# Kernel optimization log

Hardware: AMD Instinct MI355X
Metric: run time of the kernel (lower is better)

## Reference

```python
import jax, jax.numpy as jnp
import numpy as np

N = 50000
E = 800000
IN_C, HID_C, OUT_C = 128, 128, 64


def setup_inputs() -> dict:
    key = jax.random.key(0)
    k_x, k_e, k_w1, k_w2 = jax.random.split(key, 4)
    x = jax.random.normal(k_x, (N, IN_C), dtype=jnp.float32)
    edge_index = jax.random.randint(k_e, (2, E), 0, N, dtype=jnp.int64)
    # glorot-ish init scale
    W1 = jax.random.normal(k_w1, (IN_C, HID_C), dtype=jnp.float32) * (1.0 / np.sqrt(IN_C))
    b1 = jnp.zeros((HID_C,), dtype=jnp.float32)
    W2 = jax.random.normal(k_w2, (HID_C, OUT_C), dtype=jnp.float32) * (1.0 / np.sqrt(HID_C))
    b2 = jnp.zeros((OUT_C,), dtype=jnp.float32)
    return {"x": x, "edge_index": edge_index, "W1": W1, "b1": b1, "W2": W2, "b2": b2}


def _gcn_norm(edge_index, num_nodes):
    # PyG gcn_norm with add_self_loops=True: deg over destination (col), sym norm
    loops = jnp.arange(num_nodes, dtype=edge_index.dtype)
    src = jnp.concatenate([edge_index[0], loops])
    dst = jnp.concatenate([edge_index[1], loops])
    deg = jax.ops.segment_sum(jnp.ones_like(dst, dtype=jnp.float32), dst, num_segments=num_nodes)
    dinv = jnp.where(deg > 0, jax.lax.rsqrt(deg), 0.0)
    norm = dinv[src] * dinv[dst]  # [E+N]
    return src, dst, norm


def _gcn_conv(x, src, dst, norm, W, b, num_nodes):
    h = x @ W                              # [N, out]
    msg = h[src] * norm[:, None]           # [E+N, out] gather + scale
    agg = jax.ops.segment_sum(msg, dst, num_segments=num_nodes)  # scatter-add
    return agg + b


def reference(x, edge_index, W1, b1, W2, b2):
    num_nodes = x.shape[0]
    src, dst, norm = _gcn_norm(edge_index, num_nodes)
    h = _gcn_conv(x, src, dst, norm, W1, b1, num_nodes)
    h = jax.nn.relu(h)
    out = _gcn_conv(h, src, dst, norm, W2, b2, num_nodes)
    return out
```

## Files before the change

kernel.cpp:

```cpp
#include <hip/hip_runtime.h>
#include <hip/hip_bf16.h>


#define IN_C 128
#define HID_C 128
#define OUT_C 64
#define BKT_SH 8
#define BKT_NODES 256
#define CHUNK 4096
#define CAPB 6144
#define OVF_CAP 65536

typedef float f32x4 __attribute__((ext_vector_type(4)));
typedef short bf16x8 __attribute__((ext_vector_type(8)));

__device__ inline unsigned short f2bf_rtn(float f) {
  unsigned u = __float_as_uint(f);
  unsigned r = u + 0x7fffu + ((u >> 16) & 1u);
  return (unsigned short)(r >> 16);
}
__device__ inline unsigned pack_bf2(float a, float b) {
  return (unsigned)f2bf_rtn(a) | ((unsigned)f2bf_rtn(b) << 16);
}

__global__ __launch_bounds__(256) void wt_zero_kernel(
    const float* __restrict__ W1, const float* __restrict__ W2,
    short* __restrict__ w1t, short* __restrict__ w2t,
    int* __restrict__ zbase, int zints) {
  int i = blockIdx.x * 256 + threadIdx.x;
  if (i < zints) zbase[i] = 0;
  if (i < IN_C * HID_C) {
    int n = i >> 7, k = i & 127;
    w1t[i] = (short)f2bf_rtn(W1[k * HID_C + n]);
  }
  if (i < HID_C * OUT_C) {
    int n = i >> 7, k = i & 127;
    w2t[i] = (short)f2bf_rtn(W2[k * OUT_C + n]);
  }
}

__global__ __launch_bounds__(256) void phase1_bin_kernel(
    const int* __restrict__ ei, unsigned* __restrict__ pairs,
    int* __restrict__ bcnt, uint2* __restrict__ ovf, int* __restrict__ ovf_cnt,
    int* __restrict__ ovfb, int E, int K) {
  __shared__ unsigned buf[CHUNK];
  __shared__ int hist[256];
  __shared__ int lofs[256];
  __shared__ int cur[256];
  __shared__ int gbase[256];
  int t = threadIdx.x;
  int base_e = blockIdx.x * CHUNK;
  int cnt_e = E - base_e;
  if (cnt_e > CHUNK) cnt_e = CHUNK;

  hist[t] = 0;
  __syncthreads();

  for (int i = t; i < cnt_e; i += 256)
    atomicAdd(&hist[ei[E + base_e + i] >> BKT_SH], 1);
  __syncthreads();

  int v = hist[t];
  int lane = t & 63, wid = t >> 6;
  int inc = v;
  #pragma unroll
  for (int off = 1; off < 64; off <<= 1) {
    int u = __shfl_up(inc, off, 64);
    if (lane >= off) inc += u;
  }
  __shared__ int ws4[4];
  if (lane == 63) ws4[wid] = inc;
  __syncthreads();
  if (t == 0) {
    int a = ws4[0], b = ws4[1], c = ws4[2];
    ws4[0] = 0; ws4[1] = a; ws4[2] = a + b; ws4[3] = a + b + c;
  }
  __syncthreads();
  int excl = ws4[wid] + inc - v;
  lofs[t] = excl;
  cur[t] = excl;
  if (t < K && v > 0) gbase[t] = atomicAdd(&bcnt[t], v);
  __syncthreads();

  for (int i = t; i < cnt_e; i += 256) {
    int src = ei[base_e + i];
    int dst = ei[E + base_e + i];
    int b = dst >> BKT_SH;
    int pos = atomicAdd(&cur[b], 1);
    buf[pos] = (unsigned)src | ((unsigned)(dst & (BKT_NODES - 1)) << 16) |
               ((unsigned)b << 24);
  }
  __syncthreads();

  for (int i = t; i < cnt_e; i += 256) {
    unsigned w = buf[i];
    int b = w >> 24;
    int g = gbase[b] + (i - lofs[b]);
    if (g < CAPB) {
      pairs[(size_t)b * CAPB + g] = w;
    } else {
      int oi = atomicAdd(ovf_cnt, 1);
      if (oi < OVF_CAP) {
        unsigned dst = (unsigned)(b << BKT_SH) | ((w >> 16) & 0xFFu);
        ovf[oi] = make_uint2(w & 0xFFFFu, dst);
        atomicAdd(&ovfb[b], 1);
      }
    }
  }
}

__global__ __launch_bounds__(256) void bucket_scan_kernel(
    const int* __restrict__ bcnt, const int* __restrict__ ovfb,
    int* __restrict__ bucket_base, int* __restrict__ rowstart, int K, int N) {
  int t = threadIdx.x;
  int tot = 0;
  if (t < K) {
    int c = bcnt[t];
    tot = (c < CAPB ? c : CAPB) + ovfb[t];
  }
  int lane = t & 63, wid = t >> 6;
  int inc = tot;
  #pragma unroll
  for (int off = 1; off < 64; off <<= 1) {
    int u = __shfl_up(inc, off, 64);
    if (lane >= off) inc += u;
  }
  __shared__ int ws4[4];
  if (lane == 63) ws4[wid] = inc;
  __syncthreads();
  if (t == 0) {
    int a = ws4[0], b = ws4[1], c = ws4[2];
    ws4[0] = 0; ws4[1] = a; ws4[2] = a + b; ws4[3] = a + b + c;
  }
  __syncthreads();
  int excl = ws4[wid] + inc - tot;
  if (t <= K) bucket_base[t] = excl;
  if (t == K) rowstart[N] = excl;
}

__global__ __launch_bounds__(256) void phase2_csr_kernel(
    const unsigned* __restrict__ pairs, const int* __restrict__ bcnt,
    const uint2* __restrict__ ovf, const int* __restrict__ ovf_cnt,
    const int* __restrict__ bucket_base, int* __restrict__ rowstart,
    float* __restrict__ dinv, unsigned short* __restrict__ csr, int N) {
  int b = blockIdx.x;
  int t = threadIdx.x;
  __shared__ int hist[BKT_NODES];
  __shared__ int cur[BKT_NODES];
  hist[t] = 0;
  __syncthreads();

  int cnt = bcnt[b];
  if (cnt > CAPB) cnt = CAPB;
  const unsigned* reg = pairs + (size_t)b * CAPB;

  for (int i = t; i < cnt; i += 256)
    atomicAdd(&hist[(reg[i] >> 16) & 0xFFu], 1);
  int oc = *ovf_cnt;
  if (oc > OVF_CAP) oc = OVF_CAP;
  for (int i = t; i < oc; i += 256) {
    uint2 p = ovf[i];
    if ((int)(p.y >> BKT_SH) == b) atomicAdd(&hist[p.y & (BKT_NODES - 1)], 1);
  }
  __syncthreads();

  int v = hist[t];
  int lane = t & 63, wid = t >> 6;
  int inc = v;
  #pragma unroll
  for (int off = 1; off < 64; off <<= 1) {
    int u = __shfl_up(inc, off, 64);
    if (lane >= off) inc += u;
  }
  __shared__ int ws4[4];
  if (lane == 63) ws4[wid] = inc;
  __syncthreads();
  if (t == 0) {
    int a = ws4[0], bb = ws4[1], c = ws4[2];
    ws4[0] = 0; ws4[1] = a; ws4[2] = a + bb; ws4[3] = a + bb + c;
  }
  __syncthreads();
  int excl = ws4[wid] + inc - v;

  int base = bucket_base[b];
  int node = b * BKT_NODES + t;
  if (node < N) {
    rowstart[node] = base + excl;
    dinv[node] = rsqrtf((float)(v + 1));
  }
  cur[t] = base + excl;
  __syncthreads();

  for (int i = t; i < cnt; i += 256) {
    unsigned w = reg[i];
    int pos = atomicAdd(&cur[(w >> 16) & 0xFFu], 1);
    csr[pos] = (unsigned short)(w & 0xffffu);
  }
  for (int i = t; i < oc; i += 256) {
    uint2 p = ovf[i];
    if ((int)(p.y >> BKT_SH) == b) {
      int pos = atomicAdd(&cur[p.y & (BKT_NODES - 1)], 1);
      csr[pos] = (unsigned short)p.x;
    }
  }
}

template <int COUT, bool ABF16>
__global__ __launch_bounds__(256) void mfma_gemm_kernel(
    const void* __restrict__ Xv, const short* __restrict__ Wt,
    const float* __restrict__ dinv, unsigned short* __restrict__ H, int ntiles) {
  int lane = threadIdx.x & 63;
  int tile = blockIdx.x * 4 + (threadIdx.x >> 6);
  if (tile >= ntiles) return;
  constexpr int NT = COUT / 16;

  int arow = tile * 16 + (lane & 15);
  int kch = (lane >> 4) * 8;

  bf16x8 afrag[4];
  if (ABF16) {
    const bf16x8* Xb = (const bf16x8*)Xv;
    #pragma unroll
    for (int kt = 0; kt < 4; ++kt)
      afrag[kt] = Xb[(size_t)arow * 16 + (kt * 32 + kch) / 8];
  } else {
    const float4* Xf = (const float4*)Xv;
    #pragma unroll
    for (int kt = 0; kt < 4; ++kt) {
      float4 f0 = Xf[(size_t)arow * 32 + (kt * 32 + kch) / 4];
      float4 f1 = Xf[(size_t)arow * 32 + (kt * 32 + kch) / 4 + 1];
      bf16x8 a;
      a[0] = (short)f2bf_rtn(f0.x); a[1] = (short)f2bf_rtn(f0.y);
      a[2] = (short)f2bf_rtn(f0.z); a[3] = (short)f2bf_rtn(f0.w);
      a[4] = (short)f2bf_rtn(f1.x); a[5] = (short)f2bf_rtn(f1.y);
      a[6] = (short)f2bf_rtn(f1.z); a[7] = (short)f2bf_rtn(f1.w);
      afrag[kt] = a;
    }
  }

  const bf16x8* W8 = (const bf16x8*)Wt;
  f32x4 zero = {0.f, 0.f, 0.f, 0.f};
  f32x4 acc[NT];
  #pragma unroll
  for (int ct = 0; ct < NT; ++ct) acc[ct] = zero;

  #pragma unroll
  for (int ct = 0; ct < NT; ++ct) {
    int bcol = ct * 16 + (lane & 15);
    #pragma unroll
    for (int kt = 0; kt < 4; ++kt) {
      bf16x8 b = W8[bcol * 16 + (kt * 32 + kch) / 8];
      acc[ct] = __builtin_amdgcn_mfma_f32_16x16x32_bf16(afrag[kt], b, acc[ct], 0, 0, 0);
    }
  }

  int r0 = tile * 16 + (lane >> 4) * 4;
  float di[4];
  #pragma unroll
  for (int j = 0; j < 4; ++j) di[j] = dinv[r0 + j];
  #pragma unroll
  for (int ct = 0; ct < NT; ++ct) {
    #pragma unroll
    for (int j = 0; j < 4; ++j)
      H[(size_t)(r0 + j) * COUT + ct * 16 + (lane & 15)] = f2bf_rtn(acc[ct][j] * di[j]);
  }
}

template <int C, bool RELU, bool OUT_BF16>
__global__ __launch_bounds__(256) void agg_bf16_kernel(
    const unsigned short* __restrict__ Hs, const int* __restrict__ rowstart,
    const unsigned short* __restrict__ csr, const float* __restrict__ dinv,
    const float* __restrict__ bias, void* __restrict__ out, int n) {
  constexpr int TPN = C / 8;
  constexpr int NPB = 256 / TPN;
  int lane = threadIdx.x % TPN;
  int node = blockIdx.x * NPB + threadIdx.x / TPN;
  if (node >= n) return;

  const uint4* H4 = reinterpret_cast<const uint4*>(Hs);
  int s = rowstart[node];
  int e = rowstart[node + 1];

  float acc[8];
  {
    uint4 v = H4[(size_t)node * TPN + lane];
    acc[0] = __uint_as_float(v.x << 16);
    acc[1] = __uint_as_float(v.x & 0xffff0000u);
    acc[2] = __uint_as_float(v.y << 16);
    acc[3] = __uint_as_float(v.y & 0xffff0000u);
    acc[4] = __uint_as_float(v.z << 16);
    acc[5] = __uint_as_float(v.z & 0xffff0000u);
    acc[6] = __uint_as_float(v.w << 16);
    acc[7] = __uint_as_float(v.w & 0xffff0000u);
  }

  int p = s;
  for (; p + 1 < e; p += 2) {
    int s0 = csr[p];
    int s1 = csr[p + 1];
    uint4 v0 = H4[(size_t)s0 * TPN + lane];
    uint4 v1 = H4[(size_t)s1 * TPN + lane];
    acc[0] += __uint_as_float(v0.x << 16);
    acc[1] += __uint_as_float(v0.x & 0xffff0000u);
    acc[2] += __uint_as_float(v0.y << 16);
    acc[3] += __uint_as_float(v0.y & 0xffff0000u);
    acc[4] += __uint_as_float(v0.z << 16);
    acc[5] += __uint_as_float(v0.z & 0xffff0000u);
    acc[6] += __uint_as_float(v0.w << 16);
    acc[7] += __uint_as_float(v0.w & 0xffff0000u);
    acc[0] += __uint_as_float(v1.x << 16);
    acc[1] += __uint_as_float(v1.x & 0xffff0000u);
    acc[2] += __uint_as_float(v1.y << 16);
    acc[3] += __uint_as_float(v1.y & 0xffff0000u);
    acc[4] += __uint_as_float(v1.z << 16);
    acc[5] += __uint_as_float(v1.z & 0xffff0000u);
    acc[6] += __uint_as_float(v1.w << 16);
    acc[7] += __uint_as_float(v1.w & 0xffff0000u);
  }
  if (p < e) {
    int s0 = csr[p];
    uint4 v0 = H4[(size_t)s0 * TPN + lane];
    acc[0] += __uint_as_float(v0.x << 16);
    acc[1] += __uint_as_float(v0.x & 0xffff0000u);
    acc[2] += __uint_as_float(v0.y << 16);
    acc[3] += __uint_as_float(v0.y & 0xffff0000u);
    acc[4] += __uint_as_float(v0.z << 16);
    acc[5] += __uint_as_float(v0.z & 0xffff0000u);
    acc[6] += __uint_as_float(v0.w << 16);
    acc[7] += __uint_as_float(v0.w & 0xffff0000u);
  }

  float di = dinv[node];
  float4 b0 = reinterpret_cast<const float4*>(bias)[lane * 2];
  float4 b1 = reinterpret_cast<const float4*>(bias)[lane * 2 + 1];
  float r[8];
  r[0] = fmaf(acc[0], di, b0.x);
  r[1] = fmaf(acc[1], di, b0.y);
  r[2] = fmaf(acc[2], di, b0.z);
  r[3] = fmaf(acc[3], di, b0.w);
  r[4] = fmaf(acc[4], di, b1.x);
  r[5] = fmaf(acc[5], di, b1.y);
  r[6] = fmaf(acc[6], di, b1.z);
  r[7] = fmaf(acc[7], di, b1.w);
  if (RELU) {
    #pragma unroll
    for (int j = 0; j < 8; ++j) r[j] = fmaxf(r[j], 0.f);
  }
  if (OUT_BF16) {
    uint4 o;
    o.x = pack_bf2(r[0], r[1]);
    o.y = pack_bf2(r[2], r[3]);
    o.z = pack_bf2(r[4], r[5]);
    o.w = pack_bf2(r[6], r[7]);
    reinterpret_cast<uint4*>(out)[(size_t)node * TPN + lane] = o;
  } else {
    float4* o4 = reinterpret_cast<float4*>(out) + (size_t)node * (C / 4);
    o4[lane * 2] = make_float4(r[0], r[1], r[2], r[3]);
    o4[lane * 2 + 1] = make_float4(r[4], r[5], r[6], r[7]);
  }
}

extern "C" void kernel_launch(void* const* d_in, const int* in_sizes, int n_in,
                              void* d_out, int out_size, void* d_ws, size_t ws_size,
                              hipStream_t stream) {
  const float* x  = (const float*)d_in[0];
  const int*   ei = (const int*)d_in[1];
  const float* W1 = (const float*)d_in[2];
  const float* b1 = (const float*)d_in[3];
  const float* W2 = (const float*)d_in[4];
  const float* b2 = (const float*)d_in[5];
  float* out = (float*)d_out;

  const int N = in_sizes[0] / IN_C;
  const int E = in_sizes[1] / 2;
  const int K = (N + BKT_NODES - 1) >> BKT_SH;
  const int NTILES = (N + 15) / 16;

  char* ws = (char*)d_ws;
  size_t off = 0;
  auto alloc = [&](size_t bytes) -> void* {
    void* p = ws + off;
    off += (bytes + 255) & ~(size_t)255;
    return p;
  };
  int* bcnt    = (int*)alloc((size_t)K * 4);
  int* ovf_cnt = (int*)alloc(4);
  int* ovfb    = (int*)alloc((size_t)K * 4);
  size_t zero_bytes = off;
  const int zints = (int)(zero_bytes / 4);

  int*   bucket_base = (int*)  alloc((size_t)(K + 1) * 4);
  int*   rowstart    = (int*)  alloc((size_t)(N + 1) * 4);
  float* dinv        = (float*)alloc((size_t)N * 4);
  unsigned* pairs    = (unsigned*)alloc((size_t)K * CAPB * 4);
  uint2* ovf         = (uint2*)alloc((size_t)OVF_CAP * 8);
  unsigned short* csr = (unsigned short*)alloc((size_t)E * 2);
  unsigned short* hs  = (unsigned short*)alloc((size_t)N * HID_C * 2);
  unsigned short* x2  = (unsigned short*)alloc((size_t)N * HID_C * 2);
  short* w1t         = (short*)alloc((size_t)IN_C * HID_C * 2);
  short* w2t         = (short*)alloc((size_t)HID_C * OUT_C * 2);

  int wt_threads = zints > IN_C * HID_C ? zints : IN_C * HID_C;
  wt_zero_kernel<<<(wt_threads + 255) / 256, 256, 0, stream>>>(
      W1, W2, w1t, w2t, (int*)ws, zints);
  phase1_bin_kernel<<<(E + CHUNK - 1) / CHUNK, 256, 0, stream>>>(
      ei, pairs, bcnt, ovf, ovf_cnt, ovfb, E, K);
  bucket_scan_kernel<<<1, 256, 0, stream>>>(bcnt, ovfb, bucket_base, rowstart, K, N);
  phase2_csr_kernel<<<K, 256, 0, stream>>>(
      pairs, bcnt, ovf, ovf_cnt, bucket_base, rowstart, dinv, csr, N);

  mfma_gemm_kernel<HID_C, false><<<(NTILES + 3) / 4, 256, 0, stream>>>(
      x, w1t, dinv, hs, NTILES);
  agg_bf16_kernel<HID_C, true, true><<<(N + 15) / 16, 256, 0, stream>>>(
      hs, rowstart, csr, dinv, b1, x2, N);

  mfma_gemm_kernel<OUT_C, true><<<(NTILES + 3) / 4, 256, 0, stream>>>(
      x2, w2t, dinv, hs, NTILES);
  agg_bf16_kernel<OUT_C, false, false><<<(N + 31) / 32, 256, 0, stream>>>(
      hs, rowstart, csr, dinv, b2, out, N);
}
```

Before: 123.5 us.

## Slice aggregation kernels by feature columns and use nontemporal csr loads and stores

The aggregation kernels now split each node's feature row into 32-byte column slices, with consecutive blocks handling the same node range for different slices. Each block gathers only a narrow slice of H across 128 nodes. The intent is to shrink each block's gather working set and improve L2 locality. The cost is that every slice re-reads rowstart and csr. The csr loads and output stores also become nontemporal to avoid polluting the cache.

```diff
diff --git a/kernel.cpp b/kernel.cpp
--- a/kernel.cpp
+++ b/kernel.cpp
@@ -12,6 +12,7 @@
 #define OVF_CAP 65536
 
 typedef float f32x4 __attribute__((ext_vector_type(4)));
+typedef unsigned u32x4 __attribute__((ext_vector_type(4)));
 typedef short bf16x8 __attribute__((ext_vector_type(8)));
 
 __device__ inline unsigned short f2bf_rtn(float f) {
@@ -266,24 +267,27 @@
   }
 }
 
-template <int C, bool RELU, bool OUT_BF16>
-__global__ __launch_bounds__(256) void agg_bf16_kernel(
+template <int C, int SLICES, bool RELU, bool OUT_BF16>
+__global__ __launch_bounds__(256) void agg_sliced_kernel(
     const unsigned short* __restrict__ Hs, const int* __restrict__ rowstart,
     const unsigned short* __restrict__ csr, const float* __restrict__ dinv,
     const float* __restrict__ bias, void* __restrict__ out, int n) {
-  constexpr int TPN = C / 8;
-  constexpr int NPB = 256 / TPN;
-  int lane = threadIdx.x % TPN;
-  int node = blockIdx.x * NPB + threadIdx.x / TPN;
+  constexpr int ROW_U4 = C / 8;
+  static_assert(ROW_U4 / SLICES == 2, "slice must be 2 uint4 = 32B");
+  int slice = blockIdx.x % SLICES;
+  int nb = blockIdx.x / SLICES;
+  int lane = threadIdx.x & 1;
+  int node = nb * 128 + (threadIdx.x >> 1);
   if (node >= n) return;
 
-  const uint4* H4 = reinterpret_cast<const uint4*>(Hs);
+  const u32x4* H4 = reinterpret_cast<const u32x4*>(Hs);
+  int col4 = slice * 2 + lane;
   int s = rowstart[node];
   int e = rowstart[node + 1];
 
   float acc[8];
   {
-    uint4 v = H4[(size_t)node * TPN + lane];
+    u32x4 v = H4[(size_t)node * ROW_U4 + col4];
     acc[0] = __uint_as_float(v.x << 16);
     acc[1] = __uint_as_float(v.x & 0xffff0000u);
     acc[2] = __uint_as_float(v.y << 16);
@@ -296,10 +300,10 @@
 
   int p = s;
   for (; p + 1 < e; p += 2) {
-    int s0 = csr[p];
-    int s1 = csr[p + 1];
-    uint4 v0 = H4[(size_t)s0 * TPN + lane];
-    uint4 v1 = H4[(size_t)s1 * TPN + lane];
+    int s0 = __builtin_nontemporal_load(&csr[p]);
+    int s1 = __builtin_nontemporal_load(&csr[p + 1]);
+    u32x4 v0 = H4[(size_t)s0 * ROW_U4 + col4];
+    u32x4 v1 = H4[(size_t)s1 * ROW_U4 + col4];
     acc[0] += __uint_as_float(v0.x << 16);
     acc[1] += __uint_as_float(v0.x & 0xffff0000u);
     acc[2] += __uint_as_float(v0.y << 16);
@@ -318,8 +322,8 @@
     acc[7] += __uint_as_float(v1.w & 0xffff0000u);
   }
   if (p < e) {
-    int s0 = csr[p];
-    uint4 v0 = H4[(size_t)s0 * TPN + lane];
+    int s0 = __builtin_nontemporal_load(&csr[p]);
+    u32x4 v0 = H4[(size_t)s0 * ROW_U4 + col4];
     acc[0] += __uint_as_float(v0.x << 16);
     acc[1] += __uint_as_float(v0.x & 0xffff0000u);
     acc[2] += __uint_as_float(v0.y << 16);
@@ -331,8 +335,9 @@
   }
 
   float di = dinv[node];
-  float4 b0 = reinterpret_cast<const float4*>(bias)[lane * 2];
-  float4 b1 = reinterpret_cast<const float4*>(bias)[lane * 2 + 1];
+  const float4* bias4 = reinterpret_cast<const float4*>(bias);
+  float4 b0 = bias4[col4 * 2];
+  float4 b1 = bias4[col4 * 2 + 1];
   float r[8];
   r[0] = fmaf(acc[0], di, b0.x);
   r[1] = fmaf(acc[1], di, b0.y);
@@ -347,16 +352,18 @@
     for (int j = 0; j < 8; ++j) r[j] = fmaxf(r[j], 0.f);
   }
   if (OUT_BF16) {
-    uint4 o;
+    u32x4 o;
     o.x = pack_bf2(r[0], r[1]);
     o.y = pack_bf2(r[2], r[3]);
     o.z = pack_bf2(r[4], r[5]);
     o.w = pack_bf2(r[6], r[7]);
-    reinterpret_cast<uint4*>(out)[(size_t)node * TPN + lane] = o;
+    __builtin_nontemporal_store(o, reinterpret_cast<u32x4*>(out) + (size_t)node * ROW_U4 + col4);
   } else {
-    float4* o4 = reinterpret_cast<float4*>(out) + (size_t)node * (C / 4);
-    o4[lane * 2] = make_float4(r[0], r[1], r[2], r[3]);
-    o4[lane * 2 + 1] = make_float4(r[4], r[5], r[6], r[7]);
+    f32x4* o4 = reinterpret_cast<f32x4*>(out) + (size_t)node * (C / 4);
+    f32x4 r0v = {r[0], r[1], r[2], r[3]};
+    f32x4 r1v = {r[4], r[5], r[6], r[7]};
+    __builtin_nontemporal_store(r0v, o4 + col4 * 2);
+    __builtin_nontemporal_store(r1v, o4 + col4 * 2 + 1);
   }
 }
 
@@ -375,6 +382,7 @@
   const int E = in_sizes[1] / 2;
   const int K = (N + BKT_NODES - 1) >> BKT_SH;
   const int NTILES = (N + 15) / 16;
+  const int NBLK = (N + 127) / 128;
 
   char* ws = (char*)d_ws;
   size_t off = 0;
@@ -411,11 +419,11 @@
 
   mfma_gemm_kernel<HID_C, false><<<(NTILES + 3) / 4, 256, 0, stream>>>(
       x, w1t, dinv, hs, NTILES);
-  agg_bf16_kernel<HID_C, true, true><<<(N + 15) / 16, 256, 0, stream>>>(
+  agg_sliced_kernel<HID_C, 8, true, true><<<8 * NBLK, 256, 0, stream>>>(
       hs, rowstart, csr, dinv, b1, x2, N);
 
   mfma_gemm_kernel<OUT_C, true><<<(NTILES + 3) / 4, 256, 0, stream>>>(
       x2, w2t, dinv, hs, NTILES);
-  agg_bf16_kernel<OUT_C, false, false><<<(N + 31) / 32, 256, 0, stream>>>(
+  agg_sliced_kernel<OUT_C, 4, false, false><<<4 * NBLK, 256, 0, stream>>>(
       hs, rowstart, csr, dinv, b2, out, N);
 }
```

After: 234.7 us. +90.0%, slower.

## Fuse edge binning with first GEMM and fold bucket scan into CSR kernel

Applied to the files above, without the earlier changes.

The first-layer GEMM no longer pre-scales rows by dinv, so it can run in the same launch as the edge-binning phase, with blocks split by index into binning blocks and GEMM blocks. The source-side dinv scaling moves into the first aggregation as a per-edge gather of dinv[src] and an FMA. The single-block bucket scan kernel is removed, and each CSR block now recomputes the bucket prefix scan itself. Together these cut two launches and let binning and GEMM work share the GPU, at the cost of extra per-edge dinv loads in aggregation and a redundant scan in every CSR block.

```diff
diff --git a/kernel.cpp b/kernel.cpp
--- a/kernel.cpp
+++ b/kernel.cpp
@@ -39,192 +39,88 @@
   }
 }
 
-__global__ __launch_bounds__(256) void phase1_bin_kernel(
+__global__ __launch_bounds__(256) void p1_gemm1_kernel(
     const int* __restrict__ ei, unsigned* __restrict__ pairs,
     int* __restrict__ bcnt, uint2* __restrict__ ovf, int* __restrict__ ovf_cnt,
-    int* __restrict__ ovfb, int E, int K) {
-  __shared__ unsigned buf[CHUNK];
-  __shared__ int hist[256];
-  __shared__ int lofs[256];
-  __shared__ int cur[256];
-  __shared__ int gbase[256];
+    int* __restrict__ ovfb, int E, int K, int P1B,
+    const float* __restrict__ X, const short* __restrict__ Wt,
+    unsigned short* __restrict__ H, int ntiles) {
   int t = threadIdx.x;
-  int base_e = blockIdx.x * CHUNK;
-  int cnt_e = E - base_e;
-  if (cnt_e > CHUNK) cnt_e = CHUNK;
-
-  hist[t] = 0;
-  __syncthreads();
-
-  for (int i = t; i < cnt_e; i += 256)
-    atomicAdd(&hist[ei[E + base_e + i] >> BKT_SH], 1);
-  __syncthreads();
-
-  int v = hist[t];
-  int lane = t & 63, wid = t >> 6;
-  int inc = v;
-  #pragma unroll
-  for (int off = 1; off < 64; off <<= 1) {
-    int u = __shfl_up(inc, off, 64);
-    if (lane >= off) inc += u;
-  }
-  __shared__ int ws4[4];
-  if (lane == 63) ws4[wid] = inc;
-  __syncthreads();
-  if (t == 0) {
-    int a = ws4[0], b = ws4[1], c = ws4[2];
-    ws4[0] = 0; ws4[1] = a; ws4[2] = a + b; ws4[3] = a + b + c;
-  }
-  __syncthreads();
-  int excl = ws4[wid] + inc - v;
-  lofs[t] = excl;
-  cur[t] = excl;
-  if (t < K && v > 0) gbase[t] = atomicAdd(&bcnt[t], v);
-  __syncthreads();
-
-  for (int i = t; i < cnt_e; i += 256) {
-    int src = ei[base_e + i];
-    int dst = ei[E + base_e + i];
-    int b = dst >> BKT_SH;
-    int pos = atomicAdd(&cur[b], 1);
-    buf[pos] = (unsigned)src | ((unsigned)(dst & (BKT_NODES - 1)) << 16) |
-               ((unsigned)b << 24);
-  }
-  __syncthreads();
-
-  for (int i = t; i < cnt_e; i += 256) {
-    unsigned w = buf[i];
-    int b = w >> 24;
-    int g = gbase[b] + (i - lofs[b]);
-    if (g < CAPB) {
-      pairs[(size_t)b * CAPB + g] = w;
-    } else {
-      int oi = atomicAdd(ovf_cnt, 1);
-      if (oi < OVF_CAP) {
-        unsigned dst = (unsigned)(b << BKT_SH) | ((w >> 16) & 0xFFu);
-        ovf[oi] = make_uint2(w & 0xFFFFu, dst);
-        atomicAdd(&ovfb[b], 1);
+  if ((int)blockIdx.x < P1B) {
+    __shared__ unsigned buf[CHUNK];
+    __shared__ int hist[256];
+    __shared__ int lofs[256];
+    __shared__ int cur[256];
+    __shared__ int gbase[256];
+    __shared__ int ws4[4];
+    int base_e = blockIdx.x * CHUNK;
+    int cnt_e = E - base_e;
+    if (cnt_e > CHUNK) cnt_e = CHUNK;
+
+    hist[t] = 0;
+    __syncthreads();
+
+    for (int i = t; i < cnt_e; i += 256)
+      atomicAdd(&hist[ei[E + base_e + i] >> BKT_SH], 1);
+    __syncthreads();
+
+    int v = hist[t];
+    int lane = t & 63, wid = t >> 6;
+    int inc = v;
+    #pragma unroll
+    for (int off = 1; off < 64; off <<= 1) {
+      int u = __shfl_up(inc, off, 64);
+      if (lane >= off) inc += u;
+    }
+    if (lane == 63) ws4[wid] = inc;
+    __syncthreads();
+    if (t == 0) {
+      int a = ws4[0], b = ws4[1], c = ws4[2];
+      ws4[0] = 0; ws4[1] = a; ws4[2] = a + b; ws4[3] = a + b + c;
+    }
+    __syncthreads();
+    int excl = ws4[wid] + inc - v;
+    lofs[t] = excl;
+    cur[t] = excl;
+    if (t < K && v > 0) gbase[t] = atomicAdd(&bcnt[t], v);
+    __syncthreads();
+
+    for (int i = t; i < cnt_e; i += 256) {
+      int src = ei[base_e + i];
+      int dst = ei[E + base_e + i];
+      int b = dst >> BKT_SH;
+      int pos = atomicAdd(&cur[b], 1);
+      buf[pos] = (unsigned)src | ((unsigned)(dst & (BKT_NODES - 1)) << 16) |
+                 ((unsigned)b << 24);
+    }
+    __syncthreads();
+
+    for (int i = t; i < cnt_e; i += 256) {
+      unsigned w = buf[i];
+      int b = w >> 24;
+      int g = gbase[b] + (i - lofs[b]);
+      if (g < CAPB) {
+        pairs[(size_t)b * CAPB + g] = w;
+      } else {
+        int oi = atomicAdd(ovf_cnt, 1);
+        if (oi < OVF_CAP) {
+          unsigned dst = (unsigned)(b << BKT_SH) | ((w >> 16) & 0xFFu);
+          ovf[oi] = make_uint2(w & 0xFFFFu, dst);
+          atomicAdd(&ovfb[b], 1);
+        }
       }
     }
-  }
-}
-
-__global__ __launch_bounds__(256) void bucket_scan_kernel(
-    const int* __restrict__ bcnt, const int* __restrict__ ovfb,
-    int* __restrict__ bucket_base, int* __restrict__ rowstart, int K, int N) {
-  int t = threadIdx.x;
-  int tot = 0;
-  if (t < K) {
-    int c = bcnt[t];
-    tot = (c < CAPB ? c : CAPB) + ovfb[t];
-  }
-  int lane = t & 63, wid = t >> 6;
-  int inc = tot;
-  #pragma unroll
-  for (int off = 1; off < 64; off <<= 1) {
-    int u = __shfl_up(inc, off, 64);
-    if (lane >= off) inc += u;
-  }
-  __shared__ int ws4[4];
-  if (lane == 63) ws4[wid] = inc;
-  __syncthreads();
-  if (t == 0) {
-    int a = ws4[0], b = ws4[1], c = ws4[2];
-    ws4[0] = 0; ws4[1] = a; ws4[2] = a + b; ws4[3] = a + b + c;
-  }
-  __syncthreads();
-  int excl = ws4[wid] + inc - tot;
-  if (t <= K) bucket_base[t] = excl;
-  if (t == K) rowstart[N] = excl;
-}
-
-__global__ __launch_bounds__(256) void phase2_csr_kernel(
-    const unsigned* __restrict__ pairs, const int* __restrict__ bcnt,
-    const uint2* __restrict__ ovf, const int* __restrict__ ovf_cnt,
-    const int* __restrict__ bucket_base, int* __restrict__ rowstart,
-    float* __restrict__ dinv, unsigned short* __restrict__ csr, int N) {
-  int b = blockIdx.x;
-  int t = threadIdx.x;
-  __shared__ int hist[BKT_NODES];
-  __shared__ int cur[BKT_NODES];
-  hist[t] = 0;
-  __syncthreads();
-
-  int cnt = bcnt[b];
-  if (cnt > CAPB) cnt = CAPB;
-  const unsigned* reg = pairs + (size_t)b * CAPB;
-
-  for (int i = t; i < cnt; i += 256)
-    atomicAdd(&hist[(reg[i] >> 16) & 0xFFu], 1);
-  int oc = *ovf_cnt;
-  if (oc > OVF_CAP) oc = OVF_CAP;
-  for (int i = t; i < oc; i += 256) {
-    uint2 p = ovf[i];
-    if ((int)(p.y >> BKT_SH) == b) atomicAdd(&hist[p.y & (BKT_NODES - 1)], 1);
-  }
-  __syncthreads();
-
-  int v = hist[t];
-  int lane = t & 63, wid = t >> 6;
-  int inc = v;
-  #pragma unroll
-  for (int off = 1; off < 64; off <<= 1) {
-    int u = __shfl_up(inc, off, 64);
-    if (lane >= off) inc += u;
-  }
-  __shared__ int ws4[4];
-  if (lane == 63) ws4[wid] = inc;
-  __syncthreads();
-  if (t == 0) {
-    int a = ws4[0], bb = ws4[1], c = ws4[2];
-    ws4[0] = 0; ws4[1] = a; ws4[2] = a + bb; ws4[3] = a + bb + c;
-  }
-  __syncthreads();
-  int excl = ws4[wid] + inc - v;
-
-  int base = bucket_base[b];
-  int node = b * BKT_NODES + t;
-  if (node < N) {
-    rowstart[node] = base + excl;
-    dinv[node] = rsqrtf((float)(v + 1));
-  }
-  cur[t] = base + excl;
-  __syncthreads();
-
-  for (int i = t; i < cnt; i += 256) {
-    unsigned w = reg[i];
-    int pos = atomicAdd(&cur[(w >> 16) & 0xFFu], 1);
-    csr[pos] = (unsigned short)(w & 0xffffu);
-  }
-  for (int i = t; i < oc; i += 256) {
-    uint2 p = ovf[i];
-    if ((int)(p.y >> BKT_SH) == b) {
-      int pos = atomicAdd(&cur[p.y & (BKT_NODES - 1)], 1);
-      csr[pos] = (unsigned short)p.x;
-    }
-  }
-}
-
-template <int COUT, bool ABF16>
-__global__ __launch_bounds__(256) void mfma_gemm_kernel(
-    const void* __restrict__ Xv, const short* __restrict__ Wt,
-    const float* __restrict__ dinv, unsigned short* __restrict__ H, int ntiles) {
-  int lane = threadIdx.x & 63;
-  int tile = blockIdx.x * 4 + (threadIdx.x >> 6);
-  if (tile >= ntiles) return;
-  constexpr int NT = COUT / 16;
-
-  int arow = tile * 16 + (lane & 15);
-  int kch = (lane >> 4) * 8;
-
-  bf16x8 afrag[4];
-  if (ABF16) {
-    const bf16x8* Xb = (const bf16x8*)Xv;
-    #pragma unroll
-    for (int kt = 0; kt < 4; ++kt)
-      afrag[kt] = Xb[(size_t)arow * 16 + (kt * 32 + kch) / 8];
   } else {
-    const float4* Xf = (const float4*)Xv;
+    int lane = t & 63;
+    int tile = ((int)blockIdx.x - P1B) * 4 + (t >> 6);
+    if (tile >= ntiles) return;
+    constexpr int NT = HID_C / 16;
+
+    int arow = tile * 16 + (lane & 15);
+    int kch = (lane >> 4) * 8;
+
+    bf16x8 afrag[4];
+    const float4* Xf = (const float4*)X;
     #pragma unroll
     for (int kt = 0; kt < 4; ++kt) {
       float4 f0 = Xf[(size_t)arow * 32 + (kt * 32 + kch) / 4];
@@ -236,7 +132,144 @@
       a[6] = (short)f2bf_rtn(f1.z); a[7] = (short)f2bf_rtn(f1.w);
       afrag[kt] = a;
     }
-  }
+
+    const bf16x8* W8 = (const bf16x8*)Wt;
+    f32x4 zero = {0.f, 0.f, 0.f, 0.f};
+    f32x4 acc[NT];
+    #pragma unroll
+    for (int ct = 0; ct < NT; ++ct) acc[ct] = zero;
+
+    #pragma unroll
+    for (int ct = 0; ct < NT; ++ct) {
+      int bcol = ct * 16 + (lane & 15);
+      #pragma unroll
+      for (int kt = 0; kt < 4; ++kt) {
+        bf16x8 b = W8[bcol * 16 + (kt * 32 + kch) / 8];
+        acc[ct] = __builtin_amdgcn_mfma_f32_16x16x32_bf16(afrag[kt], b, acc[ct], 0, 0, 0);
+      }
+    }
+
+    int r0 = tile * 16 + (lane >> 4) * 4;
+    #pragma unroll
+    for (int ct = 0; ct < NT; ++ct) {
+      #pragma unroll
+      for (int j = 0; j < 4; ++j)
+        H[(size_t)(r0 + j) * HID_C + ct * 16 + (lane & 15)] = f2bf_rtn(acc[ct][j]);
+    }
+  }
+}
+
+__global__ __launch_bounds__(256) void phase2_csr_kernel(
+    const unsigned* __restrict__ pairs, const int* __restrict__ bcnt,
+    const int* __restrict__ ovfb, const uint2* __restrict__ ovf,
+    const int* __restrict__ ovf_cnt, int* __restrict__ rowstart,
+    float* __restrict__ dinv, unsigned short* __restrict__ csr, int N, int K) {
+  int b = blockIdx.x;
+  int t = threadIdx.x;
+  __shared__ int hist[BKT_NODES];
+  __shared__ int cur[BKT_NODES];
+  __shared__ int sbase[256];
+  __shared__ int ws4[4];
+  int lane = t & 63, wid = t >> 6;
+
+  int cb = 0;
+  if (t < K) {
+    int c = bcnt[t];
+    cb = (c < CAPB ? c : CAPB) + ovfb[t];
+  }
+  {
+    int inc = cb;
+    #pragma unroll
+    for (int off = 1; off < 64; off <<= 1) {
+      int u = __shfl_up(inc, off, 64);
+      if (lane >= off) inc += u;
+    }
+    if (lane == 63) ws4[wid] = inc;
+    __syncthreads();
+    if (t == 0) {
+      int a = ws4[0], bb = ws4[1], c = ws4[2];
+      ws4[0] = 0; ws4[1] = a; ws4[2] = a + bb; ws4[3] = a + bb + c;
+    }
+    __syncthreads();
+    int excl = ws4[wid] + inc - cb;
+    sbase[t] = excl;
+    if (b == K - 1 && t == K - 1) rowstart[N] = excl + cb;
+  }
+  __syncthreads();
+  int base = sbase[b];
+
+  hist[t] = 0;
+  __syncthreads();
+
+  int cnt = bcnt[b];
+  if (cnt > CAPB) cnt = CAPB;
+  const unsigned* reg = pairs + (size_t)b * CAPB;
+
+  for (int i = t; i < cnt; i += 256)
+    atomicAdd(&hist[(reg[i] >> 16) & 0xFFu], 1);
+  int oc = *ovf_cnt;
+  if (oc > OVF_CAP) oc = OVF_CAP;
+  for (int i = t; i < oc; i += 256) {
+    uint2 p = ovf[i];
+    if ((int)(p.y >> BKT_SH) == b) atomicAdd(&hist[p.y & (BKT_NODES - 1)], 1);
+  }
+  __syncthreads();
+
+  int v = hist[t];
+  int inc = v;
+  #pragma unroll
+  for (int off = 1; off < 64; off <<= 1) {
+    int u = __shfl_up(inc, off, 64);
+    if (lane >= off) inc += u;
+  }
+  __syncthreads();
+  if (lane == 63) ws4[wid] = inc;
+  __syncthreads();
+  if (t == 0) {
+    int a = ws4[0], bb = ws4[1], c = ws4[2];
+    ws4[0] = 0; ws4[1] = a; ws4[2] = a + bb; ws4[3] = a + bb + c;
+  }
+  __syncthreads();
+  int excl = ws4[wid] + inc - v;
+
+  int node = b * BKT_NODES + t;
+  if (node < N) {
+    rowstart[node] = base + excl;
+    dinv[node] = rsqrtf((float)(v + 1));
+  }
+  cur[t] = base + excl;
+  __syncthreads();
+
+  for (int i = t; i < cnt; i += 256) {
+    unsigned w = reg[i];
+    int pos = atomicAdd(&cur[(w >> 16) & 0xFFu], 1);
+    csr[pos] = (unsigned short)(w & 0xffffu);
+  }
+  for (int i = t; i < oc; i += 256) {
+    uint2 p = ovf[i];
+    if ((int)(p.y >> BKT_SH) == b) {
+      int pos = atomicAdd(&cur[p.y & (BKT_NODES - 1)], 1);
+      csr[pos] = (unsigned short)p.x;
+    }
+  }
+}
+
+__global__ __launch_bounds__(256) void mfma_gemm2_kernel(
+    const unsigned short* __restrict__ Xb16, const short* __restrict__ Wt,
+    const float* __restrict__ dinv, unsigned short* __restrict__ H, int ntiles) {
+  int lane = threadIdx.x & 63;
+  int tile = blockIdx.x * 4 + (threadIdx.x >> 6);
+  if (tile >= ntiles) return;
+  constexpr int NT = OUT_C / 16;
+
+  int arow = tile * 16 + (lane & 15);
+  int kch = (lane >> 4) * 8;
+
+  const bf16x8* Xb = (const bf16x8*)Xb16;
+  bf16x8 afrag[4];
+  #pragma unroll
+  for (int kt = 0; kt < 4; ++kt)
+    afrag[kt] = Xb[(size_t)arow * 16 + (kt * 32 + kch) / 8];
 
   const bf16x8* W8 = (const bf16x8*)Wt;
   f32x4 zero = {0.f, 0.f, 0.f, 0.f};
@@ -262,11 +295,11 @@
   for (int ct = 0; ct < NT; ++ct) {
     #pragma unroll
     for (int j = 0; j < 4; ++j)
-      H[(size_t)(r0 + j) * COUT + ct * 16 + (lane & 15)] = f2bf_rtn(acc[ct][j] * di[j]);
-  }
-}
-
-template <int C, bool RELU, bool OUT_BF16>
+      H[(size_t)(r0 + j) * OUT_C + ct * 16 + (lane & 15)] = f2bf_rtn(acc[ct][j] * di[j]);
+  }
+}
+
+template <int C, bool RELU, bool OUT_BF16, bool SRC_SCALE>
 __global__ __launch_bounds__(256) void agg_bf16_kernel(
     const unsigned short* __restrict__ Hs, const int* __restrict__ rowstart,
     const unsigned short* __restrict__ csr, const float* __restrict__ dinv,
@@ -280,18 +313,20 @@
   const uint4* H4 = reinterpret_cast<const uint4*>(Hs);
   int s = rowstart[node];
   int e = rowstart[node + 1];
+  float dnode = dinv[node];
 
   float acc[8];
   {
     uint4 v = H4[(size_t)node * TPN + lane];
-    acc[0] = __uint_as_float(v.x << 16);
-    acc[1] = __uint_as_float(v.x & 0xffff0000u);
-    acc[2] = __uint_as_float(v.y << 16);
-    acc[3] = __uint_as_float(v.y & 0xffff0000u);
-    acc[4] = __uint_as_float(v.z << 16);
-    acc[5] = __uint_as_float(v.z & 0xffff0000u);
-    acc[6] = __uint_as_float(v.w << 16);
-    acc[7] = __uint_as_float(v.w & 0xffff0000u);
+    float ds = SRC_SCALE ? dnode : 1.0f;
+    acc[0] = __uint_as_float(v.x << 16) * ds;
+    acc[1] = __uint_as_float(v.x & 0xffff0000u) * ds;
+    acc[2] = __uint_as_float(v.y << 16) * ds;
+    acc[3] = __uint_as_float(v.y & 0xffff0000u) * ds;
+    acc[4] = __uint_as_float(v.z << 16) * ds;
+    acc[5] = __uint_as_float(v.z & 0xffff0000u) * ds;
+    acc[6] = __uint_as_float(v.w << 16) * ds;
+    acc[7] = __uint_as_float(v.w & 0xffff0000u) * ds;
   }
 
   int p = s;
@@ -300,48 +335,68 @@
     int s1 = csr[p + 1];
     uint4 v0 = H4[(size_t)s0 * TPN + lane];
     uint4 v1 = H4[(size_t)s1 * TPN + lane];
-    acc[0] += __uint_as_float(v0.x << 16);
-    acc[1] += __uint_as_float(v0.x & 0xffff0000u);
-    acc[2] += __uint_as_float(v0.y << 16);
-    acc[3] += __uint_as_float(v0.y & 0xffff0000u);
-    acc[4] += __uint_as_float(v0.z << 16);
-    acc[5] += __uint_as_float(v0.z & 0xffff0000u);
-    acc[6] += __uint_as_float(v0.w << 16);
-    acc[7] += __uint_as_float(v0.w & 0xffff0000u);
-    acc[0] += __uint_as_float(v1.x << 16);
-    acc[1] += __uint_as_float(v1.x & 0xffff0000u);
-    acc[2] += __uint_as_float(v1.y << 16);
-    acc[3] += __uint_as_float(v1.y & 0xffff0000u);
-    acc[4] += __uint_as_float(v1.z << 16);
-    acc[5] += __uint_as_float(v1.z & 0xffff0000u);
-    acc[6] += __uint_as_float(v1.w << 16);
-    acc[7] += __uint_as_float(v1.w & 0xffff0000u);
+    if (SRC_SCALE) {
+      float d0 = dinv[s0], d1 = dinv[s1];
+      acc[0] = fmaf(__uint_as_float(v0.x << 16), d0, acc[0]);
+      acc[1] = fmaf(__uint_as_float(v0.x & 0xffff0000u), d0, acc[1]);
+      acc[2] = fmaf(__uint_as_float(v0.y << 16), d0, acc[2]);
+      acc[3] = fmaf(__uint_as_float(v0.y & 0xffff0000u), d0, acc[3]);
+      acc[4] = fmaf(__uint_as_float(v0.z << 16), d0, acc[4]);
+      acc[5] = fmaf(__uint_as_float(v0.z & 0xffff0000u), d0, acc[5]);
+      acc[6] = fmaf(__uint_as_float(v0.w << 16), d0, acc[6]);
+      acc[7] = fmaf(__uint_as_float(v0.w & 0xffff0000u), d0, acc[7]);
+      acc[0] = fmaf(__uint_as_float(v1.x << 16), d1, acc[0]);
+      acc[1] = fmaf(__uint_as_float(v1.x & 0xffff0000u), d1, acc[1]);
+      acc[2] = fmaf(__uint_as_float(v1.y << 16), d1, acc[2]);
+      acc[3] = fmaf(__uint_as_float(v1.y & 0xffff0000u), d1, acc[3]);
+      acc[4] = fmaf(__uint_as_float(v1.z << 16), d1, acc[4]);
+      acc[5] = fmaf(__uint_as_float(v1.z & 0xffff0000u), d1, acc[5]);
+      acc[6] = fmaf(__uint_as_float(v1.w << 16), d1, acc[6]);
+      acc[7] = fmaf(__uint_as_float(v1.w & 0xffff0000u), d1, acc[7]);
+    } else {
+      acc[0] += __uint_as_float(v0.x << 16);
+      acc[1] += __uint_as_float(v0.x & 0xffff0000u);
+      acc[2] += __uint_as_float(v0.y << 16);
+      acc[3] += __uint_as_float(v0.y & 0xffff0000u);
+      acc[4] += __uint_as_float(v0.z << 16);
+      acc[5] += __uint_as_float(v0.z & 0xffff0000u);
+      acc[6] += __uint_as_float(v0.w << 16);
+      acc[7] += __uint_as_float(v0.w & 0xffff0000u);
+      acc[0] += __uint_as_float(v1.x << 16);
+      acc[1] += __uint_as_float(v1.x & 0xffff0000u);
+      acc[2] += __uint_as_float(v1.y << 16);
+      acc[3] += __uint_as_float(v1.y & 0xffff0000u);
+      acc[4] += __uint_as_float(v1.z << 16);
+      acc[5] += __uint_as_float(v1.z & 0xffff0000u);
+      acc[6] += __uint_as_float(v1.w << 16);
+      acc[7] += __uint_as_float(v1.w & 0xffff0000u);
+    }
   }
   if (p < e) {
     int s0 = csr[p];
     uint4 v0 = H4[(size_t)s0 * TPN + lane];
-    acc[0] += __uint_as_float(v0.x << 16);
-    acc[1] += __uint_as_float(v0.x & 0xffff0000u);
-    acc[2] += __uint_as_float(v0.y << 16);
-    acc[3] += __uint_as_float(v0.y & 0xffff0000u);
-    acc[4] += __uint_as_float(v0.z << 16);
-    acc[5] += __uint_as_float(v0.z & 0xffff0000u);
-    acc[6] += __uint_as_float(v0.w << 16);
-    acc[7] += __uint_as_float(v0.w & 0xffff0000u);
-  }
-
-  float di = dinv[node];
+    float d0 = SRC_SCALE ? dinv[s0] : 1.0f;
+    acc[0] = fmaf(__uint_as_float(v0.x << 16), d0, acc[0]);
+    acc[1] = fmaf(__uint_as_float(v0.x & 0xffff0000u), d0, acc[1]);
+    acc[2] = fmaf(__uint_as_float(v0.y << 16), d0, acc[2]);
+    acc[3] = fmaf(__uint_as_float(v0.y & 0xffff0000u), d0, acc[3]);
+    acc[4] = fmaf(__uint_as_float(v0.z << 16), d0, acc[4]);
+    acc[5] = fmaf(__uint_as_float(v0.z & 0xffff0000u), d0, acc[5]);
+    acc[6] = fmaf(__uint_as_float(v0.w << 16), d0, acc[6]);
+    acc[7] = fmaf(__uint_as_float(v0.w & 0xffff0000u), d0, acc[7]);
+  }
+
   float4 b0 = reinterpret_cast<const float4*>(bias)[lane * 2];
   float4 b1 = reinterpret_cast<const float4*>(bias)[lane * 2 + 1];
   float r[8];
-  r[0] = fmaf(acc[0], di, b0.x);
-  r[1] = fmaf(acc[1], di, b0.y);
-  r[2] = fmaf(acc[2], di, b0.z);
-  r[3] = fmaf(acc[3], di, b0.w);
-  r[4] = fmaf(acc[4], di, b1.x);
-  r[5] = fmaf(acc[5], di, b1.y);
-  r[6] = fmaf(acc[6], di, b1.z);
-  r[7] = fmaf(acc[7], di, b1.w);
+  r[0] = fmaf(acc[0], dnode, b0.x);
+  r[1] = fmaf(acc[1], dnode, b0.y);
+  r[2] = fmaf(acc[2], dnode, b0.z);
+  r[3] = fmaf(acc[3], dnode, b0.w);
+  r[4] = fmaf(acc[4], dnode, b1.x);
+  r[5] = fmaf(acc[5], dnode, b1.y);
+  r[6] = fmaf(acc[6], dnode, b1.z);
+  r[7] = fmaf(acc[7], dnode, b1.w);
   if (RELU) {
     #pragma unroll
     for (int j = 0; j < 8; ++j) r[j] = fmaxf(r[j], 0.f);
@@ -375,6 +430,8 @@
   const int E = in_sizes[1] / 2;
   const int K = (N + BKT_NODES - 1) >> BKT_SH;
   const int NTILES = (N + 15) / 16;
+  const int P1B = (E + CHUNK - 1) / CHUNK;
+  const int GB1 = (NTILES + 3) / 4;
 
   char* ws = (char*)d_ws;
   size_t off = 0;
@@ -389,7 +446,6 @@
   size_t zero_bytes = off;
   const int zints = (int)(zero_bytes / 4);
 
-  int*   bucket_base = (int*)  alloc((size_t)(K + 1) * 4);
   int*   rowstart    = (int*)  alloc((size_t)(N + 1) * 4);
   float* dinv        = (float*)alloc((size_t)N * 4);
   unsigned* pairs    = (unsigned*)alloc((size_t)K * CAPB * 4);
@@ -403,19 +459,19 @@
   int wt_threads = zints > IN_C * HID_C ? zints : IN_C * HID_C;
   wt_zero_kernel<<<(wt_threads + 255) / 256, 256, 0, stream>>>(
       W1, W2, w1t, w2t, (int*)ws, zints);
-  phase1_bin_kernel<<<(E + CHUNK - 1) / CHUNK, 256, 0, stream>>>(
-      ei, pairs, bcnt, ovf, ovf_cnt, ovfb, E, K);
-  bucket_scan_kernel<<<1, 256, 0, stream>>>(bcnt, ovfb, bucket_base, rowstart, K, N);
+
+  p1_gemm1_kernel<<<P1B + GB1, 256, 0, stream>>>(
+      ei, pairs, bcnt, ovf, ovf_cnt, ovfb, E, K, P1B, x, w1t, hs, NTILES);
+
   phase2_csr_kernel<<<K, 256, 0, stream>>>(
-      pairs, bcnt, ovf, ovf_cnt, bucket_base, rowstart, dinv, csr, N);
-
-  mfma_gemm_kernel<HID_C, false><<<(NTILES + 3) / 4, 256, 0, stream>>>(
-      x, w1t, dinv, hs, NTILES);
-  agg_bf16_kernel<HID_C, true, true><<<(N + 15) / 16, 256, 0, stream>>>(
+      pairs, bcnt, ovfb, ovf, ovf_cnt, rowstart, dinv, csr, N, K);
+
+  agg_bf16_kernel<HID_C, true, true, true><<<(N + 15) / 16, 256, 0, stream>>>(
       hs, rowstart, csr, dinv, b1, x2, N);
 
-  mfma_gemm_kernel<OUT_C, true><<<(NTILES + 3) / 4, 256, 0, stream>>>(
+  mfma_gemm2_kernel<<<(NTILES + 3) / 4, 256, 0, stream>>>(
       x2, w2t, dinv, hs, NTILES);
-  agg_bf16_kernel<OUT_C, false, false><<<(N + 31) / 32, 256, 0, stream>>>(
+
+  agg_bf16_kernel<OUT_C, false, false, false><<<(N + 31) / 32, 256, 0, stream>>>(
       hs, rowstart, csr, dinv, b2, out, N);
 }
```

Measured after the change: 110.5 us. -10.6%, faster.
